# Kernel optimization log

Hardware: AMD Instinct MI355X
Metric: run time of the kernel (lower is better)

Reference implementation:

```python
import jax, jax.numpy as jnp
import numpy as np

B, L, H, W = 4, 5000, 256, 256
C_IN, DIM_LOI, N_PTS0, N_PTS1, DIM_FC, N_OUT_LINE = 256, 128, 32, 8, 1024, 2500
SCALE = N_PTS0 // N_PTS1  # MaxPool1d kernel/stride


def setup_inputs() -> dict:
    key = jax.random.key(0)
    ks = jax.random.split(key, 8)
    feature = jax.random.normal(ks[0], (B, C_IN, H, W), jnp.float32)
    # line endpoints in pixel coords of the 256x256 feature map
    lines = jax.random.uniform(ks[1], (B, L, 2, 2), jnp.float32) * (H - 1)
    s = lambda fan: 1.0 / np.sqrt(fan)
    fc1_w = (jax.random.normal(ks[2], (DIM_LOI, C_IN), jnp.float32) * s(C_IN))
    fc1_b = jnp.zeros((DIM_LOI,), jnp.float32)
    w1 = jax.random.normal(ks[3], (DIM_LOI * N_PTS1, DIM_FC), jnp.float32) * s(DIM_LOI * N_PTS1)
    b1 = jnp.zeros((DIM_FC,), jnp.float32)
    w2 = jax.random.normal(ks[4], (DIM_FC, DIM_FC), jnp.float32) * s(DIM_FC)
    b2 = jnp.zeros((DIM_FC,), jnp.float32)
    w3 = jax.random.normal(ks[5], (DIM_FC, 4), jnp.float32) * s(DIM_FC)
    b3 = jnp.zeros((4,), jnp.float32)
    return dict(feature=feature, lines=lines, fc1_w=fc1_w, fc1_b=fc1_b,
                w1=w1, b1=b1, w2=w2, b2=b2, w3=w3, b3=b3)


def reference(feature, lines, fc1_w, fc1_b, w1, b1, w2, b2, w3, b3):
    # fc1: 1x1 conv  [B,C_IN,H,W] -> [B,DIM_LOI,H,W]
    x = jnp.einsum('bchw,oc->bohw', feature, fc1_w) + fc1_b[None, :, None, None]

    # sample N_PTS0 points along each line (lerp between endpoints), minus 0.5
    lam = jnp.linspace(0.0, 1.0, N_PTS0, dtype=feature.dtype)[None, None, :, None]
    p = lines[:, :, 0:1, :] * lam + lines[:, :, 1:2, :] * (1.0 - lam) - 0.5  # [B,L,P,2]
    px, py = p[..., 0], p[..., 1]  # px indexes H (rows), py indexes W (cols)
    px0 = jnp.clip(jnp.floor(px), 0.0, H - 1.0)
    py0 = jnp.clip(jnp.floor(py), 0.0, W - 1.0)
    px1 = jnp.clip(px0 + 1.0, 0.0, H - 1.0)
    py1 = jnp.clip(py0 + 1.0, 0.0, W - 1.0)
    ix0, iy0 = px0.astype(jnp.int32), py0.astype(jnp.int32)
    ix1, iy1 = px1.astype(jnp.int32), py1.astype(jnp.int32)
    idx00 = ix0 * W + iy0
    idx10 = ix1 * W + iy0
    idx01 = ix0 * W + iy1
    idx11 = ix1 * W + iy1
    w00 = (px1 - px) * (py1 - py)
    w10 = (px - px0) * (py1 - py)
    w01 = (px1 - px) * (py - py0)
    w11 = (px - px0) * (py - py0)

    def gather_one(fmap, i00, i10, i01, i11, g00, g10, g01, g11):
        f = fmap.reshape(DIM_LOI, H * W)
        g = lambda idx: f[:, idx.reshape(-1)].reshape(DIM_LOI, L, N_PTS0)
        return g(i00) * g00 + g(i10) * g10 + g(i01) * g01 + g(i11) * g11

    xp = jax.vmap(gather_one)(x, idx00, idx10, idx01, idx11, w00, w10, w01, w11)
    # xp: [B, DIM_LOI, L, N_PTS0] -> maxpool along points -> [B, DIM_LOI, L, N_PTS1]
    xp = xp.reshape(B, DIM_LOI, L, N_PTS1, SCALE).max(-1)
    # reshape like torch: [N, DIM_LOI, N_PTS1] -> [N, DIM_LOI*N_PTS1] (channel-major)
    feat = xp.transpose(0, 2, 1, 3).reshape(B, L, DIM_LOI * N_PTS1)

    # fc2 MLP -> 4 logits
    h = jax.nn.relu(feat @ w1 + b1)
    h = jax.nn.relu(h @ w2 + b2)
    logits = h @ w3 + b3  # [B, L, 4]
    s = jax.nn.softmax(logits, axis=-1)

    # threshold conditions
    keep = ((s[..., 1] > 0.25) | (s[..., 2] > 0.25) | (s[..., 3] > 0.25)) & (s[..., 0] < 0.25)

    def select(p0, s0, m):
        cnt = m.sum()
        key = jnp.where(m, jnp.argmax(s0, -1), -1)  # masked-out get -1 -> sorted last
        order = jnp.argsort(-key)  # stable desc sort of argmax class
        idx = order[jnp.arange(N_OUT_LINE) % jnp.maximum(cnt, 1)]
        lo = jnp.where(cnt > 0, p0[idx], 0.0)
        so = jnp.where(cnt > 0, s0[idx], 0.0)
        return lo, so

    lines_out, score_out = jax.vmap(select)(lines, s, keep)
    return lines_out, score_out, s
```

## Files before the change

kernel.cpp:

```cpp
#include <hip/hip_runtime.h>
#include <cstdint>
#include <cstddef>

#define B_     4
#define L_     5000
#define H_     256
#define W_     256
#define HW_    65536
#define CIN_   256
#define DLOI_  128
#define NPTS0_ 32
#define NPTS1_ 8
#define DFC_   1024
#define NOUT_  2500
#define M_     (B_*L_)
#define MPAD_  20096

typedef _Float16 f16;
typedef _Float16 f16x4 __attribute__((ext_vector_type(4)));
typedef _Float16 f16x8 __attribute__((ext_vector_type(8)));
typedef float    f32x4 __attribute__((ext_vector_type(4)));

__device__ __forceinline__ void gload16(const void* g, void* l) {
  __builtin_amdgcn_global_load_lds(
      (const __attribute__((address_space(1))) void*)g,
      (__attribute__((address_space(3))) void*)l, 16, 0, 0);
}

__global__ __launch_bounds__(256) void k_wsplit(const float* __restrict__ src,
                                                f16* __restrict__ h,
                                                f16* __restrict__ l) {
  int i = (blockIdx.x * 256 + threadIdx.x) * 4;
  float4 v = *(const float4*)(src + i);
  f16 h0 = (f16)v.x, h1 = (f16)v.y, h2 = (f16)v.z, h3 = (f16)v.w;
  *(f16x4*)(h + i) = (f16x4){h0, h1, h2, h3};
  *(f16x4*)(l + i) = (f16x4){(f16)(v.x - (float)h0), (f16)(v.y - (float)h1),
                             (f16)(v.z - (float)h2), (f16)(v.w - (float)h3)};
}

__global__ __launch_bounds__(256) void k_conv_mfma(const float* __restrict__ fin,
                                                   const f16* __restrict__ wh,
                                                   const f16* __restrict__ wl,
                                                   const float* __restrict__ bias,
                                                   float* __restrict__ xout) {
  __shared__ f16 lds[16384];
  const int t = threadIdx.x;
  const int P0 = blockIdx.x * 128;
  const int b  = P0 >> 16;
  const int ph0 = P0 & 65535;
  const int lane = t & 63, wave = t >> 6;
  const int quad = lane >> 4, lo = lane & 15;
  const int wm = wave >> 1, wn = wave & 1;

  const int c_base = (t & 7) * 4;
  const int p = (t >> 3) * 4;
  const size_t fbase = (size_t)b * CIN_ * HW_ + (size_t)ph0 + p;

  const int srow = t >> 2;
  const int skb  = (t & 3) * 16;
  const char* gBh = (const char*)wh + (size_t)srow * 512 + skb;
  const char* gBl = (const char*)wl + (size_t)srow * 512 + skb;
  char* ldsB = (char*)lds + t * 16;

  f32x4 acc[4][4];
  #pragma unroll
  for (int mt = 0; mt < 4; mt++)
    #pragma unroll
    for (int nt = 0; nt < 4; nt++) acc[mt][nt] = (f32x4){0.f, 0.f, 0.f, 0.f};

  float4 av[4], nv[4];
  #pragma unroll
  for (int j = 0; j < 4; j++)
    av[j] = *(const float4*)(fin + fbase + (size_t)(c_base + j) * HW_);

  for (int kc = 0; kc < 8; kc++) {
    const size_t bko = (size_t)kc * 64;
    gload16(gBh + bko,         ldsB + 16384);
    gload16(gBh + 32768 + bko, ldsB + 16384 + 4096);
    gload16(gBl + bko,         ldsB + 24576);
    gload16(gBl + 32768 + bko, ldsB + 24576 + 4096);

    #pragma unroll
    for (int i = 0; i < 4; i++) {
      f16 hh[4], ll[4];
      #pragma unroll
      for (int j = 0; j < 4; j++) {
        float v = ((const float*)&av[j])[i];
        hh[j] = (f16)v;
        ll[j] = (f16)(v - (float)hh[j]);
      }
      *(f16x4*)(&lds[(p + i) * 32 + c_base])        = (f16x4){hh[0], hh[1], hh[2], hh[3]};
      *(f16x4*)(&lds[4096 + (p + i) * 32 + c_base]) = (f16x4){ll[0], ll[1], ll[2], ll[3]};
    }
    __syncthreads();

    if (kc < 7) {
      #pragma unroll
      for (int j = 0; j < 4; j++)
        nv[j] = *(const float4*)(fin + fbase + (size_t)((kc + 1) * 32 + c_base + j) * HW_);
    }

    f16x8 ah[4], al[4], bh4[4], bl4[4];
    #pragma unroll
    for (int mt = 0; mt < 4; mt++) {
      int row = wm * 64 + mt * 16 + lo;
      ah[mt] = *(const f16x8*)(&lds[row * 32 + quad * 8]);
      al[mt] = *(const f16x8*)(&lds[4096 + row * 32 + quad * 8]);
    }
    #pragma unroll
    for (int nt = 0; nt < 4; nt++) {
      int row = wn * 64 + nt * 16 + lo;
      bh4[nt] = *(const f16x8*)(&lds[8192 + row * 32 + quad * 8]);
      bl4[nt] = *(const f16x8*)(&lds[12288 + row * 32 + quad * 8]);
    }
    #pragma unroll
    for (int mt = 0; mt < 4; mt++)
      #pragma unroll
      for (int nt = 0; nt < 4; nt++) {
        acc[mt][nt] = __builtin_amdgcn_mfma_f32_16x16x32_f16(ah[mt], bh4[nt], acc[mt][nt], 0, 0, 0);
        acc[mt][nt] = __builtin_amdgcn_mfma_f32_16x16x32_f16(ah[mt], bl4[nt], acc[mt][nt], 0, 0, 0);
        acc[mt][nt] = __builtin_amdgcn_mfma_f32_16x16x32_f16(al[mt], bh4[nt], acc[mt][nt], 0, 0, 0);
      }
    __syncthreads();
    #pragma unroll
    for (int j = 0; j < 4; j++) av[j] = nv[j];
  }

  #pragma unroll
  for (int nt = 0; nt < 4; nt++) {
    int col = wn * 64 + nt * 16 + lo;
    float bv = bias[col];
    #pragma unroll
    for (int mt = 0; mt < 4; mt++) {
      int rowb = P0 + wm * 64 + mt * 16 + quad * 4;
      #pragma unroll
      for (int r = 0; r < 4; r++)
        xout[(size_t)(rowb + r) * DLOI_ + col] = acc[mt][nt][r] + bv;
    }
  }
}

__global__ __launch_bounds__(128) void k_sample(const float* __restrict__ x,
                                                const float* __restrict__ lines,
                                                f16* __restrict__ fh,
                                                f16* __restrict__ fl) {
  const int blk = blockIdx.x;
  const int b = blk / L_;
  const int c = threadIdx.x;
  const float* ln = lines + (size_t)blk * 4;
  const float e0x = ln[0], e0y = ln[1], e1x = ln[2], e1y = ln[3];
  const float* xb = x + (size_t)b * HW_ * DLOI_;
  f16x8 vh, vl;
  for (int q = 0; q < NPTS1_; q++) {
    float m = -1e30f;
    #pragma unroll
    for (int r = 0; r < 4; r++) {
      int i = q * 4 + r;
      float lam = (float)i * (1.0f / 31.0f);
      float px = e0x * lam + e1x * (1.f - lam) - 0.5f;
      float py = e0y * lam + e1y * (1.f - lam) - 0.5f;
      float px0 = fminf(fmaxf(floorf(px), 0.f), 255.f);
      float py0 = fminf(fmaxf(floorf(py), 0.f), 255.f);
      float px1 = fminf(px0 + 1.f, 255.f);
      float py1 = fminf(py0 + 1.f, 255.f);
      int ix0 = (int)px0, iy0 = (int)py0, ix1 = (int)px1, iy1 = (int)py1;
      float w00 = (px1 - px) * (py1 - py);
      float w10 = (px - px0) * (py1 - py);
      float w01 = (px1 - px) * (py - py0);
      float w11 = (px - px0) * (py - py0);
      float v = w00 * xb[(size_t)(ix0 * W_ + iy0) * DLOI_ + c]
              + w10 * xb[(size_t)(ix1 * W_ + iy0) * DLOI_ + c]
              + w01 * xb[(size_t)(ix0 * W_ + iy1) * DLOI_ + c]
              + w11 * xb[(size_t)(ix1 * W_ + iy1) * DLOI_ + c];
      m = fmaxf(m, v);
    }
    f16 h = (f16)m;
    vh[q] = h;
    vl[q] = (f16)(m - (float)h);
  }
  *(f16x8*)(fh + (size_t)blk * DFC_ + c * 8) = vh;
  *(f16x8*)(fl + (size_t)blk * DFC_ + c * 8) = vl;
}

__global__ __launch_bounds__(256) void k_tsplit(const float* __restrict__ Wsrc,
                                                f16* __restrict__ Th,
                                                f16* __restrict__ Tl) {
  __shared__ float tile[32][33];
  const int bj = blockIdx.x, bi = blockIdx.y;
  const int tx = threadIdx.x & 31, ty = threadIdx.x >> 5;
  #pragma unroll
  for (int r = ty; r < 32; r += 8)
    tile[r][tx] = Wsrc[(size_t)(bi * 32 + r) * 1024 + bj * 32 + tx];
  __syncthreads();
  #pragma unroll
  for (int r = ty; r < 32; r += 8) {
    float v = tile[tx][r];
    f16 h = (f16)v;
    size_t o = (size_t)(bj * 32 + r) * 1024 + bi * 32 + tx;
    Th[o] = h;
    Tl[o] = (f16)(v - (float)h);
  }
}

template <bool SPLIT_OUT>
__global__ __launch_bounds__(256) void k_gemm_f16x3(
    const f16* __restrict__ Ah, const f16* __restrict__ Al,
    const f16* __restrict__ Bh, const f16* __restrict__ Bl,
    const float* __restrict__ bias,
    f16* __restrict__ Oh, f16* __restrict__ Ol, float* __restrict__ Of,
    int M) {
  constexpr int K = DFC_;
  __shared__ f16 lds[16384];
  const int t = threadIdx.x;
  const int n0 = blockIdx.x * 128;
  const int r0 = blockIdx.y * 128;
  const int lane = t & 63, wave = t >> 6;
  const int quad = lane >> 4, lo = lane & 15;
  const int wm = wave >> 1, wn = wave & 1;

  const int srow = t >> 2;
  const int skb  = (t & 3) * 16;
  const char* gA_h = (const char*)Ah + (size_t)(r0 + srow) * (K * 2) + skb;
  const char* gA_l = (const char*)Al + (size_t)(r0 + srow) * (K * 2) + skb;
  const char* gB_h = (const char*)Bh + (size_t)(n0 + srow) * (K * 2) + skb;
  const char* gB_l = (const char*)Bl + (size_t)(n0 + srow) * (K * 2) + skb;
  char* lb = (char*)lds + t * 16;
  const size_t rstride64 = (size_t)64 * K * 2;

  f32x4 acc[4][4];
  #pragma unroll
  for (int mt = 0; mt < 4; mt++)
    #pragma unroll
    for (int nt = 0; nt < 4; nt++) acc[mt][nt] = (f32x4){0.f, 0.f, 0.f, 0.f};

  for (int kc = 0; kc < K / 32; kc++) {
    const size_t go = (size_t)kc * 64;
    gload16(gA_h + go,             lb);
    gload16(gA_h + rstride64 + go, lb + 4096);
    gload16(gA_l + go,             lb + 8192);
    gload16(gA_l + rstride64 + go, lb + 12288);
    gload16(gB_h + go,             lb + 16384);
    gload16(gB_h + rstride64 + go, lb + 20480);
    gload16(gB_l + go,             lb + 24576);
    gload16(gB_l + rstride64 + go, lb + 28672);
    __syncthreads();

    f16x8 ah[4], al[4], bh[4], bl[4];
    #pragma unroll
    for (int mt = 0; mt < 4; mt++) {
      int row = wm * 64 + mt * 16 + lo;
      ah[mt] = *(const f16x8*)(lds + row * 32 + quad * 8);
      al[mt] = *(const f16x8*)(lds + 4096 + row * 32 + quad * 8);
    }
    #pragma unroll
    for (int nt = 0; nt < 4; nt++) {
      int row = wn * 64 + nt * 16 + lo;
      bh[nt] = *(const f16x8*)(lds + 8192 + row * 32 + quad * 8);
      bl[nt] = *(const f16x8*)(lds + 12288 + row * 32 + quad * 8);
    }
    #pragma unroll
    for (int mt = 0; mt < 4; mt++)
      #pragma unroll
      for (int nt = 0; nt < 4; nt++) {
        acc[mt][nt] = __builtin_amdgcn_mfma_f32_16x16x32_f16(ah[mt], bh[nt], acc[mt][nt], 0, 0, 0);
        acc[mt][nt] = __builtin_amdgcn_mfma_f32_16x16x32_f16(ah[mt], bl[nt], acc[mt][nt], 0, 0, 0);
        acc[mt][nt] = __builtin_amdgcn_mfma_f32_16x16x32_f16(al[mt], bh[nt], acc[mt][nt], 0, 0, 0);
      }
    __syncthreads();
  }

  #pragma unroll
  for (int mt = 0; mt < 4; mt++)
    #pragma unroll
    for (int nt = 0; nt < 4; nt++) {
      int col = n0 + wn * 64 + nt * 16 + lo;
      float bv = bias[col];
      int rowb = r0 + wm * 64 + mt * 16 + quad * 4;
      #pragma unroll
      for (int r = 0; r < 4; r++) {
        int row = rowb + r;
        if (row < M) {
          float v = fmaxf(acc[mt][nt][r] + bv, 0.f);
          if (SPLIT_OUT) {
            f16 h = (f16)v;
            Oh[(size_t)row * DFC_ + col] = h;
            Ol[(size_t)row * DFC_ + col] = (f16)(v - (float)h);
          } else {
            Of[(size_t)row * DFC_ + col] = v;
          }
        }
      }
    }
}

__global__ __launch_bounds__(256) void k_head(const float* __restrict__ h2,
                                              const float* __restrict__ w3,
                                              const float* __restrict__ b3,
                                              float* __restrict__ s_out,
                                              int* __restrict__ key_out) {
  const int wave = threadIdx.x >> 6;
  const int lane = threadIdx.x & 63;
  const int row = blockIdx.x * 4 + wave;
  if (row >= M_) return;
  const float* hr = h2 + (size_t)row * DFC_;
  float a0 = 0.f, a1 = 0.f, a2 = 0.f, a3 = 0.f;
  for (int k = lane; k < DFC_; k += 64) {
    float hv = hr[k];
    float4 wv = *(const float4*)(w3 + k * 4);
    a0 = fmaf(hv, wv.x, a0);
    a1 = fmaf(hv, wv.y, a1);
    a2 = fmaf(hv, wv.z, a2);
    a3 = fmaf(hv, wv.w, a3);
  }
  #pragma unroll
  for (int off = 32; off >= 1; off >>= 1) {
    a0 += __shfl_down(a0, off);
    a1 += __shfl_down(a1, off);
    a2 += __shfl_down(a2, off);
    a3 += __shfl_down(a3, off);
  }
  if (lane == 0) {
    float l0 = a0 + b3[0], l1 = a1 + b3[1], l2 = a2 + b3[2], l3 = a3 + b3[3];
    float mx = fmaxf(fmaxf(l0, l1), fmaxf(l2, l3));
    float e0 = expf(l0 - mx), e1 = expf(l1 - mx), e2 = expf(l2 - mx), e3 = expf(l3 - mx);
    float inv = 1.f / (e0 + e1 + e2 + e3);
    float s0 = e0 * inv, s1 = e1 * inv, s2 = e2 * inv, s3 = e3 * inv;
    *(float4*)(s_out + (size_t)row * 4) = make_float4(s0, s1, s2, s3);
    bool keep = ((s1 > 0.25f) || (s2 > 0.25f) || (s3 > 0.25f)) && (s0 < 0.25f);
    int am = 0; float best = s0;
    if (s1 > best) { best = s1; am = 1; }
    if (s2 > best) { best = s2; am = 2; }
    if (s3 > best) { best = s3; am = 3; }
    key_out[row] = keep ? am : -1;
  }
}

__global__ __launch_bounds__(1024) void k_select(const int* __restrict__ key,
                                                 const float* __restrict__ lines,
                                                 const float* __restrict__ s,
                                                 float* __restrict__ out_lines,
                                                 float* __restrict__ out_score) {
  __shared__ int s_ord[L_];
  __shared__ int s_scan[1024];
  __shared__ int s_tot[5];
  const int b = blockIdx.x;
  const int t = threadIdx.x;
  const int base_l = t * 5;
  int cls[5];
  int c[5] = {0, 0, 0, 0, 0};
  #pragma unroll
  for (int i = 0; i < 5; i++) {
    int l = base_l + i;
    int cl = -1;
    if (l < L_) {
      int k = key[b * L_ + l];
      cl = (k < 0) ? 4 : (3 - k);
      c[cl]++;
    }
    cls[i] = cl;
  }
  int pf[5];
  for (int cc = 0; cc < 5; cc++) {
    s_scan[t] = c[cc];
    __syncthreads();
    for (int off = 1; off < 1024; off <<= 1) {
      int add = (t >= off) ? s_scan[t - off] : 0;
      __syncthreads();
      s_scan[t] += add;
      __syncthreads();
    }
    pf[cc] = s_scan[t] - c[cc];
    if (t == 1023) s_tot[cc] = s_scan[1023];
    __syncthreads();
  }
  int basec[5];
  basec[0] = 0;
  #pragma unroll
  for (int cc = 1; cc < 5; cc++) basec[cc] = basec[cc - 1] + s_tot[cc - 1];
  int run[5] = {0, 0, 0, 0, 0};
  #pragma unroll
  for (int i = 0; i < 5; i++) {
    if (cls[i] >= 0) {
      int cl = cls[i];
      int pos = basec[cl] + pf[cl] + run[cl];
      run[cl]++;
      s_ord[pos] = base_l + i;
    }
  }
  const int cnt = L_ - s_tot[4];
  __syncthreads();
  for (int j = t; j < NOUT_; j += 1024) {
    float4 lv = make_float4(0.f, 0.f, 0.f, 0.f);
    float4 sv = make_float4(0.f, 0.f, 0.f, 0.f);
    if (cnt > 0) {
      int idx = s_ord[j % cnt];
      lv = *(const float4*)(lines + (size_t)(b * L_ + idx) * 4);
      sv = *(const float4*)(s + (size_t)(b * L_ + idx) * 4);
    }
    *(float4*)(out_lines + (size_t)(b * NOUT_ + j) * 4) = lv;
    *(float4*)(out_score + (size_t)(b * NOUT_ + j) * 4) = sv;
  }
}

extern "C" void kernel_launch(void* const* d_in, const int* in_sizes, int n_in,
                              void* d_out, int out_size, void* d_ws, size_t ws_size,
                              hipStream_t stream) {
  const float* feature = (const float*)d_in[0];
  const float* lines   = (const float*)d_in[1];
  const float* fc1_w   = (const float*)d_in[2];
  const float* fc1_b   = (const float*)d_in[3];
  const float* w1      = (const float*)d_in[4];
  const float* b1      = (const float*)d_in[5];
  const float* w2      = (const float*)d_in[6];
  const float* b2      = (const float*)d_in[7];
  const float* w3      = (const float*)d_in[8];
  const float* b3      = (const float*)d_in[9];

  float* out_lines = (float*)d_out;
  float* out_score = out_lines + B_ * NOUT_ * 4;
  float* s_out     = out_score + B_ * NOUT_ * 4;

  char* ws = (char*)d_ws;
  float* x    = (float*)(ws);
  f16*   h1h  = (f16*)(ws);
  f16*   h1l  = (f16*)(ws + 41156608ull);
  f16*   fh   = (f16*)(ws + 134217728ull);
  f16*   fl   = (f16*)(ws + 134217728ull + 41156608ull);
  float* h2   = (float*)(ws + 134217728ull);
  f16*   wt1h = (f16*)(ws + 216530944ull);
  f16*   wt1l = (f16*)(ws + 216530944ull + 2097152ull);
  f16*   wt2h = (f16*)(ws + 216530944ull + 2ull * 2097152ull);
  f16*   wt2l = (f16*)(ws + 216530944ull + 3ull * 2097152ull);
  int*   keys = (int*)(ws + 224919552ull);
  f16*   wc_h = (f16*)(ws + 224999552ull);
  f16*   wc_l = (f16*)(ws + 224999552ull + 65536ull);

  k_wsplit<<<dim3(32), 256, 0, stream>>>(fc1_w, wc_h, wc_l);
  k_tsplit<<<dim3(32, 32), 256, 0, stream>>>(w1, wt1h, wt1l);
  k_tsplit<<<dim3(32, 32), 256, 0, stream>>>(w2, wt2h, wt2l);
  k_conv_mfma<<<dim3((B_ * HW_) / 128), 256, 0, stream>>>(feature, wc_h, wc_l, fc1_b, x);
  k_sample<<<dim3(M_), 128, 0, stream>>>(x, lines, fh, fl);
  k_gemm_f16x3<true><<<dim3(8, MPAD_ / 128), 256, 0, stream>>>(
      fh, fl, wt1h, wt1l, b1, h1h, h1l, nullptr, M_);
  k_gemm_f16x3<false><<<dim3(8, MPAD_ / 128), 256, 0, stream>>>(
      h1h, h1l, wt2h, wt2l, b2, nullptr, nullptr, h2, M_);
  k_head<<<dim3(M_ / 4), 256, 0, stream>>>(h2, w3, b3, s_out, keys);
  k_select<<<dim3(B_), 1024, 0, stream>>>(keys, lines, s_out, out_lines, out_score);
}
```

Measured before the change: 953.9 us.

## Fuse final linear head into second GEMM epilogue and remap blocks per XCD

The second GEMM no longer writes the full fp32 h2 activation. Its epilogue applies ReLU, multiplies by w3 and reduces across lanes, then writes 16 partial logit slots per row. A small head kernel sums the partials and does the softmax and keep/argmax step. Both GEMMs also switch to a 1D grid whose block index is remapped so each XCD gets a contiguous band of row tiles, which should improve L2 reuse of the A rows. This removes about 80MB of h2 writes and reads, at the cost of extra shuffles in the epilogue and some idle blocks from grid padding.

After: 888.3 us. 6.9% less time.

```diff
diff --git a/kernel.cpp b/kernel.cpp
--- a/kernel.cpp
+++ b/kernel.cpp
@@ -15,6 +15,7 @@
 #define NOUT_  2500
 #define M_     (B_*L_)
 #define MPAD_  20096
+#define NBAND_ 157
 
 typedef _Float16 f16;
 typedef _Float16 f16x4 __attribute__((ext_vector_type(4)));
@@ -207,13 +208,19 @@
     const f16* __restrict__ Ah, const f16* __restrict__ Al,
     const f16* __restrict__ Bh, const f16* __restrict__ Bl,
     const float* __restrict__ bias,
-    f16* __restrict__ Oh, f16* __restrict__ Ol, float* __restrict__ Of,
-    int M) {
+    f16* __restrict__ Oh, f16* __restrict__ Ol,
+    const float* __restrict__ w3, float* __restrict__ part) {
   constexpr int K = DFC_;
   __shared__ f16 lds[16384];
+  const int bid = blockIdx.x;
+  const int xcd = bid & 7;
+  const int t8  = bid >> 3;
+  const int nb  = t8 & 7;
+  const int rb  = xcd * 20 + (t8 >> 3);
+  if (rb >= NBAND_) return;
+  const int n0 = nb * 128;
+  const int r0 = rb * 128;
   const int t = threadIdx.x;
-  const int n0 = blockIdx.x * 128;
-  const int r0 = blockIdx.y * 128;
   const int lane = t & 63, wave = t >> 6;
   const int quad = lane >> 4, lo = lane & 15;
   const int wm = wave >> 1, wn = wave & 1;
@@ -269,70 +276,91 @@
     __syncthreads();
   }
 
-  #pragma unroll
-  for (int mt = 0; mt < 4; mt++)
-    #pragma unroll
-    for (int nt = 0; nt < 4; nt++) {
-      int col = n0 + wn * 64 + nt * 16 + lo;
-      float bv = bias[col];
-      int rowb = r0 + wm * 64 + mt * 16 + quad * 4;
-      #pragma unroll
-      for (int r = 0; r < 4; r++) {
-        int row = rowb + r;
-        if (row < M) {
-          float v = fmaxf(acc[mt][nt][r] + bv, 0.f);
-          if (SPLIT_OUT) {
+  if (SPLIT_OUT) {
+    #pragma unroll
+    for (int mt = 0; mt < 4; mt++)
+      #pragma unroll
+      for (int nt = 0; nt < 4; nt++) {
+        int col = n0 + wn * 64 + nt * 16 + lo;
+        float bv = bias[col];
+        int rowb = r0 + wm * 64 + mt * 16 + quad * 4;
+        #pragma unroll
+        for (int r = 0; r < 4; r++) {
+          int row = rowb + r;
+          if (row < M_) {
+            float v = fmaxf(acc[mt][nt][r] + bv, 0.f);
             f16 h = (f16)v;
             Oh[(size_t)row * DFC_ + col] = h;
             Ol[(size_t)row * DFC_ + col] = (f16)(v - (float)h);
-          } else {
-            Of[(size_t)row * DFC_ + col] = v;
           }
         }
       }
-    }
-}
-
-__global__ __launch_bounds__(256) void k_head(const float* __restrict__ h2,
-                                              const float* __restrict__ w3,
-                                              const float* __restrict__ b3,
-                                              float* __restrict__ s_out,
-                                              int* __restrict__ key_out) {
-  const int wave = threadIdx.x >> 6;
-  const int lane = threadIdx.x & 63;
-  const int row = blockIdx.x * 4 + wave;
+  } else {
+    const int slot = nb * 2 + wn;
+    #pragma unroll
+    for (int mt = 0; mt < 4; mt++) {
+      float p[4][4];
+      #pragma unroll
+      for (int r = 0; r < 4; r++)
+        #pragma unroll
+        for (int j = 0; j < 4; j++) p[r][j] = 0.f;
+      #pragma unroll
+      for (int nt = 0; nt < 4; nt++) {
+        int col = n0 + wn * 64 + nt * 16 + lo;
+        float bv = bias[col];
+        float4 wv = *(const float4*)(w3 + col * 4);
+        #pragma unroll
+        for (int r = 0; r < 4; r++) {
+          float v = fmaxf(acc[mt][nt][r] + bv, 0.f);
+          p[r][0] = fmaf(v, wv.x, p[r][0]);
+          p[r][1] = fmaf(v, wv.y, p[r][1]);
+          p[r][2] = fmaf(v, wv.z, p[r][2]);
+          p[r][3] = fmaf(v, wv.w, p[r][3]);
+        }
+      }
+      #pragma unroll
+      for (int r = 0; r < 4; r++)
+        #pragma unroll
+        for (int j = 0; j < 4; j++) {
+          p[r][j] += __shfl_xor(p[r][j], 1);
+          p[r][j] += __shfl_xor(p[r][j], 2);
+          p[r][j] += __shfl_xor(p[r][j], 4);
+          p[r][j] += __shfl_xor(p[r][j], 8);
+        }
+      if (lo == 0) {
+        int rowb = r0 + wm * 64 + mt * 16 + quad * 4;
+        #pragma unroll
+        for (int r = 0; r < 4; r++)
+          *(float4*)(part + ((size_t)slot * MPAD_ + rowb + r) * 4) =
+              make_float4(p[r][0], p[r][1], p[r][2], p[r][3]);
+      }
+    }
+  }
+}
+
+__global__ __launch_bounds__(256) void k_head2(const float* __restrict__ part,
+                                               const float* __restrict__ b3,
+                                               float* __restrict__ s_out,
+                                               int* __restrict__ key_out) {
+  const int row = blockIdx.x * 256 + threadIdx.x;
   if (row >= M_) return;
-  const float* hr = h2 + (size_t)row * DFC_;
-  float a0 = 0.f, a1 = 0.f, a2 = 0.f, a3 = 0.f;
-  for (int k = lane; k < DFC_; k += 64) {
-    float hv = hr[k];
-    float4 wv = *(const float4*)(w3 + k * 4);
-    a0 = fmaf(hv, wv.x, a0);
-    a1 = fmaf(hv, wv.y, a1);
-    a2 = fmaf(hv, wv.z, a2);
-    a3 = fmaf(hv, wv.w, a3);
-  }
-  #pragma unroll
-  for (int off = 32; off >= 1; off >>= 1) {
-    a0 += __shfl_down(a0, off);
-    a1 += __shfl_down(a1, off);
-    a2 += __shfl_down(a2, off);
-    a3 += __shfl_down(a3, off);
-  }
-  if (lane == 0) {
-    float l0 = a0 + b3[0], l1 = a1 + b3[1], l2 = a2 + b3[2], l3 = a3 + b3[3];
-    float mx = fmaxf(fmaxf(l0, l1), fmaxf(l2, l3));
-    float e0 = expf(l0 - mx), e1 = expf(l1 - mx), e2 = expf(l2 - mx), e3 = expf(l3 - mx);
-    float inv = 1.f / (e0 + e1 + e2 + e3);
-    float s0 = e0 * inv, s1 = e1 * inv, s2 = e2 * inv, s3 = e3 * inv;
-    *(float4*)(s_out + (size_t)row * 4) = make_float4(s0, s1, s2, s3);
-    bool keep = ((s1 > 0.25f) || (s2 > 0.25f) || (s3 > 0.25f)) && (s0 < 0.25f);
-    int am = 0; float best = s0;
-    if (s1 > best) { best = s1; am = 1; }
-    if (s2 > best) { best = s2; am = 2; }
-    if (s3 > best) { best = s3; am = 3; }
-    key_out[row] = keep ? am : -1;
-  }
+  float l0 = b3[0], l1 = b3[1], l2 = b3[2], l3 = b3[3];
+  #pragma unroll
+  for (int sl = 0; sl < 16; sl++) {
+    float4 p = *(const float4*)(part + ((size_t)sl * MPAD_ + row) * 4);
+    l0 += p.x; l1 += p.y; l2 += p.z; l3 += p.w;
+  }
+  float mx = fmaxf(fmaxf(l0, l1), fmaxf(l2, l3));
+  float e0 = expf(l0 - mx), e1 = expf(l1 - mx), e2 = expf(l2 - mx), e3 = expf(l3 - mx);
+  float inv = 1.f / (e0 + e1 + e2 + e3);
+  float s0 = e0 * inv, s1 = e1 * inv, s2 = e2 * inv, s3 = e3 * inv;
+  *(float4*)(s_out + (size_t)row * 4) = make_float4(s0, s1, s2, s3);
+  bool keep = ((s1 > 0.25f) || (s2 > 0.25f) || (s3 > 0.25f)) && (s0 < 0.25f);
+  int am = 0; float best = s0;
+  if (s1 > best) { best = s1; am = 1; }
+  if (s2 > best) { best = s2; am = 2; }
+  if (s3 > best) { best = s3; am = 3; }
+  key_out[row] = keep ? am : -1;
 }
 
 __global__ __launch_bounds__(1024) void k_select(const int* __restrict__ key,
@@ -424,9 +452,9 @@
   float* x    = (float*)(ws);
   f16*   h1h  = (f16*)(ws);
   f16*   h1l  = (f16*)(ws + 41156608ull);
+  float* part = (float*)(ws + 82313216ull);
   f16*   fh   = (f16*)(ws + 134217728ull);
   f16*   fl   = (f16*)(ws + 134217728ull + 41156608ull);
-  float* h2   = (float*)(ws + 134217728ull);
   f16*   wt1h = (f16*)(ws + 216530944ull);
   f16*   wt1l = (f16*)(ws + 216530944ull + 2097152ull);
   f16*   wt2h = (f16*)(ws + 216530944ull + 2ull * 2097152ull);
@@ -440,10 +468,10 @@
   k_tsplit<<<dim3(32, 32), 256, 0, stream>>>(w2, wt2h, wt2l);
   k_conv_mfma<<<dim3((B_ * HW_) / 128), 256, 0, stream>>>(feature, wc_h, wc_l, fc1_b, x);
   k_sample<<<dim3(M_), 128, 0, stream>>>(x, lines, fh, fl);
-  k_gemm_f16x3<true><<<dim3(8, MPAD_ / 128), 256, 0, stream>>>(
-      fh, fl, wt1h, wt1l, b1, h1h, h1l, nullptr, M_);
-  k_gemm_f16x3<false><<<dim3(8, MPAD_ / 128), 256, 0, stream>>>(
-      h1h, h1l, wt2h, wt2l, b2, nullptr, nullptr, h2, M_);
-  k_head<<<dim3(M_ / 4), 256, 0, stream>>>(h2, w3, b3, s_out, keys);
+  k_gemm_f16x3<true><<<dim3(1280), 256, 0, stream>>>(
+      fh, fl, wt1h, wt1l, b1, h1h, h1l, nullptr, nullptr);
+  k_gemm_f16x3<false><<<dim3(1280), 256, 0, stream>>>(
+      h1h, h1l, wt2h, wt2l, b2, nullptr, nullptr, w3, part);
+  k_head2<<<dim3((M_ + 255) / 256), 256, 0, stream>>>(part, b3, s_out, keys);
   k_select<<<dim3(B_), 1024, 0, stream>>>(keys, lines, s_out, out_lines, out_score);
 }
```
